# Kernel tuning notes

Hardware: AMD Instinct MI355X
Metric: run time of the kernel (lower is better)

Reference implementation:

```python
import jax, jax.numpy as jnp
import numpy as np

B = 4096        # batch (number of bags)
L = 64          # num_lookups per bag
NT = 4          # number of embedding tables
V = 500000      # rows per table
D = 128         # emb_dim
DENSE = 512     # dense feature dim
BOT = [512, 1024, 512, 128]
TOP = [D * (1 + NT), 1024, 512, 1]  # [640, 1024, 512, 1]


def _linear_params(key, dims):
    params = []
    for i in range(len(dims) - 1):
        din, dout = dims[i], dims[i + 1]
        kw, kb, key = jax.random.split(key, 3)
        sw = np.sqrt(2.0 / (din + dout)).astype(np.float32)
        sb = np.sqrt(1.0 / dout).astype(np.float32)
        params.append((sw * jax.random.normal(kw, (dout, din), jnp.float32),
                       sb * jax.random.normal(kb, (dout,), jnp.float32)))
    return params


def setup_inputs() -> dict:
    key = jax.random.key(0)
    k_dense, k_idx, k_tab, k_bot, k_top = jax.random.split(key, 5)
    inp = {}
    inp["x_dense"] = jax.random.normal(k_dense, (B, DENSE), jnp.float32)
    bound = float(np.sqrt(1.0 / V))
    inp["tables"] = jax.random.uniform(k_tab, (NT, V, D), jnp.float32, -bound, bound)
    bot = _linear_params(k_bot, BOT)
    top = _linear_params(k_top, TOP)
    inp["bw0"], inp["bb0"] = bot[0]
    inp["bw1"], inp["bb1"] = bot[1]
    inp["bw2"], inp["bb2"] = bot[2]
    inp["tw0"], inp["tb0"] = top[0]
    inp["tw1"], inp["tb1"] = top[1]
    inp["tw2"], inp["tb2"] = top[2]
    inp["x_indices"] = jax.random.randint(k_idx, (B * L, NT), 0, V, dtype=jnp.int32)
    inp["constant_offsets"] = jnp.arange(B, dtype=jnp.int32) * L  # offsets of each bag
    return inp


def reference(x_dense, tables, bw0, bb0, bw1, bb1, bw2, bb2,
              tw0, tb0, tw1, tb1, tw2, tb2, x_indices, constant_offsets):
    # bottom MLP: Linear+ReLU x3
    h = jax.nn.relu(x_dense @ bw0.T + bb0)
    h = jax.nn.relu(h @ bw1.T + bb1)
    bot_out = jax.nn.relu(h @ bw2.T + bb2)                     # [B, D]

    # EmbeddingBag (sum mode) per table, driven by offsets
    N = x_indices.shape[0]
    seg = jnp.searchsorted(constant_offsets, jnp.arange(N, dtype=constant_offsets.dtype),
                           side='right') - 1                    # [N] bag id per index
    gathered = jax.vmap(lambda tab, idx: tab[idx])(tables, x_indices.T)  # [NT, N, D]
    pooled = jax.vmap(lambda e: jax.ops.segment_sum(e, seg, num_segments=B))(gathered)  # [NT, B, D]

    # concat order: bottom MLP out, then tables 1..4 (columns 0..3)
    feat = jnp.concatenate([bot_out] + [pooled[t] for t in range(NT)], axis=1)  # [B, 640]

    # top MLP: ReLU, ReLU, Sigmoid
    z = jax.nn.relu(feat @ tw0.T + tb0)
    z = jax.nn.relu(z @ tw1.T + tb1)
    out = jax.nn.sigmoid(z @ tw2.T + tb2)                       # [B, 1]
    return out
```

## Files before the change

kernel.cpp:

```cpp
#include <hip/hip_runtime.h>
#include <hip/hip_bf16.h>
#include <cstdint>

#define B_BAGS 4096
#define L_LOOK 64
#define NT 4
#define V_ROWS 500000
#define D_EMB 128
#define FEAT 640

typedef _Float16 half8 __attribute__((ext_vector_type(8)));
typedef _Float16 half4 __attribute__((ext_vector_type(4)));
typedef float f32x4 __attribute__((ext_vector_type(4)));

#define GLOAD_LDS(g, l) __builtin_amdgcn_global_load_lds( \
    (const __attribute__((address_space(1))) void*)(g),   \
    (__attribute__((address_space(3))) void*)(l), 16, 0, 0)

template<int BM, int BN, bool RELU>
__device__ __forceinline__ void gemm_body(
    _Float16* lds, int bm, int bn,
    const _Float16* __restrict__ X, int ldx,
    const _Float16* __restrict__ W, int ldw,
    const float* __restrict__ bias,
    _Float16* __restrict__ Y, int ldy, int K)
{
    constexpr int BK = 64;
    constexpr int FM = BM / 32;
    constexpr int FN = BN / 32;
    constexpr int AI = BM * 8 / 256;
    constexpr int BI = BN * 8 / 256;

    _Float16* As = lds;
    _Float16* Bs = lds + BM * BK;

    const int tid  = threadIdx.x;
    const int lane = tid & 63;
    const int wave = tid >> 6;
    const int wm   = wave >> 1;
    const int wn   = wave & 1;
    const int q    = lane >> 4;
    const int r16  = lane & 15;

    f32x4 acc[FM][FN] = {};

    for (int k0 = 0; k0 < K; k0 += BK) {
#pragma unroll
        for (int i = 0; i < AI; ++i) {
            int L = i * 256 + tid;
            int row = L >> 3, sl = L & 7;
            const _Float16* src = X + (size_t)(bm + row) * ldx + k0 + ((sl ^ (row & 7)) * 8);
            GLOAD_LDS(src, As + (size_t)(i * 256 + wave * 64) * 8);
        }
#pragma unroll
        for (int j = 0; j < BI; ++j) {
            int L = j * 256 + tid;
            int row = L >> 3, sl = L & 7;
            const _Float16* src = W + (size_t)(bn + row) * ldw + k0 + ((sl ^ (row & 7)) * 8);
            GLOAD_LDS(src, Bs + (size_t)(j * 256 + wave * 64) * 8);
        }
        __syncthreads();

#pragma unroll
        for (int s = 0; s < 2; ++s) {
            half8 a[FM], b[FN];
#pragma unroll
            for (int i = 0; i < FM; ++i) {
                int R = wm * (BM / 2) + i * 16 + r16;
                int sl = (s * 4 + q) ^ (R & 7);
                a[i] = *(const half8*)(As + R * BK + sl * 8);
            }
#pragma unroll
            for (int j = 0; j < FN; ++j) {
                int R = wn * (BN / 2) + j * 16 + r16;
                int sl = (s * 4 + q) ^ (R & 7);
                b[j] = *(const half8*)(Bs + R * BK + sl * 8);
            }
#pragma unroll
            for (int i = 0; i < FM; ++i)
#pragma unroll
                for (int j = 0; j < FN; ++j)
                    acc[i][j] = __builtin_amdgcn_mfma_f32_16x16x32_f16(
                        a[i], b[j], acc[i][j], 0, 0, 0);
        }
        __syncthreads();
    }

#pragma unroll
    for (int i = 0; i < FM; ++i) {
        const int m0 = bm + wm * (BM / 2) + i * 16 + q * 4;
#pragma unroll
        for (int j = 0; j < FN; ++j) {
            const int n = bn + wn * (BN / 2) + j * 16 + r16;
            const float bv = bias[n];
#pragma unroll
            for (int e = 0; e < 4; ++e) {
                float o = acc[i][j][e] + bv;
                if (RELU) o = fmaxf(o, 0.f);
                Y[(size_t)(m0 + e) * ldy + n] = (_Float16)o;
            }
        }
    }
}

template<int BM, int BN, bool RELU>
__device__ __forceinline__ void gemm_body_f32(
    _Float16* lds, int bm, int bn,
    const float* __restrict__ X, int ldx,
    const float* __restrict__ W, int ldw,
    const float* __restrict__ bias,
    _Float16* __restrict__ Y, int ldy, int K)
{
    constexpr int BK = 64;
    constexpr int FM = BM / 32;
    constexpr int FN = BN / 32;
    constexpr int AI = BM * 8 / 256;
    constexpr int BI = BN * 8 / 256;

    _Float16* As = lds;
    _Float16* Bs = lds + BM * BK;

    const int tid  = threadIdx.x;
    const int lane = tid & 63;
    const int wave = tid >> 6;
    const int wm   = wave >> 1;
    const int wn   = wave & 1;
    const int q    = lane >> 4;
    const int r16  = lane & 15;

    f32x4 acc[FM][FN] = {};

    for (int k0 = 0; k0 < K; k0 += BK) {
#pragma unroll
        for (int i = 0; i < AI; ++i) {
            int S = i * 256 + tid;
            int row = S >> 3, c = S & 7;
            const float* src = X + (size_t)(bm + row) * ldx + k0 + c * 8;
            float4 v0 = *(const float4*)src;
            float4 v1 = *(const float4*)(src + 4);
            half8 h = { (_Float16)v0.x, (_Float16)v0.y, (_Float16)v0.z, (_Float16)v0.w,
                        (_Float16)v1.x, (_Float16)v1.y, (_Float16)v1.z, (_Float16)v1.w };
            *(half8*)(As + row * BK + ((c ^ (row & 7)) * 8)) = h;
        }
#pragma unroll
        for (int j = 0; j < BI; ++j) {
            int S = j * 256 + tid;
            int row = S >> 3, c = S & 7;
            const float* src = W + (size_t)(bn + row) * ldw + k0 + c * 8;
            float4 v0 = *(const float4*)src;
            float4 v1 = *(const float4*)(src + 4);
            half8 h = { (_Float16)v0.x, (_Float16)v0.y, (_Float16)v0.z, (_Float16)v0.w,
                        (_Float16)v1.x, (_Float16)v1.y, (_Float16)v1.z, (_Float16)v1.w };
            *(half8*)(Bs + row * BK + ((c ^ (row & 7)) * 8)) = h;
        }
        __syncthreads();

#pragma unroll
        for (int s = 0; s < 2; ++s) {
            half8 a[FM], b[FN];
#pragma unroll
            for (int i = 0; i < FM; ++i) {
                int R = wm * (BM / 2) + i * 16 + r16;
                int sl = (s * 4 + q) ^ (R & 7);
                a[i] = *(const half8*)(As + R * BK + sl * 8);
            }
#pragma unroll
            for (int j = 0; j < FN; ++j) {
                int R = wn * (BN / 2) + j * 16 + r16;
                int sl = (s * 4 + q) ^ (R & 7);
                b[j] = *(const half8*)(Bs + R * BK + sl * 8);
            }
#pragma unroll
            for (int i = 0; i < FM; ++i)
#pragma unroll
                for (int j = 0; j < FN; ++j)
                    acc[i][j] = __builtin_amdgcn_mfma_f32_16x16x32_f16(
                        a[i], b[j], acc[i][j], 0, 0, 0);
        }
        __syncthreads();
    }

#pragma unroll
    for (int i = 0; i < FM; ++i) {
        const int m0 = bm + wm * (BM / 2) + i * 16 + q * 4;
#pragma unroll
        for (int j = 0; j < FN; ++j) {
            const int n = bn + wn * (BN / 2) + j * 16 + r16;
            const float bv = bias[n];
#pragma unroll
            for (int e = 0; e < 4; ++e) {
                float o = acc[i][j][e] + bv;
                if (RELU) o = fmaxf(o, 0.f);
                Y[(size_t)(m0 + e) * ldy + n] = (_Float16)o;
            }
        }
    }
}

__device__ __forceinline__ void emb_body(
    int bag,
    const float* __restrict__ tables,
    const int*   __restrict__ idx,
    _Float16*    __restrict__ feat)
{
    const int wave = threadIdx.x >> 6;
    const int lane = threadIdx.x & 63;
    const int l5   = lane >> 5;
    const int c    = lane & 31;

    const int my_idx = idx[((size_t)bag * L_LOOK + lane) * NT + wave];
    const float* tab = tables + (size_t)wave * V_ROWS * D_EMB;

    float4 acc = {0.f, 0.f, 0.f, 0.f};
#pragma unroll 16
    for (int j = 0; j < 32; ++j) {
        int r = __shfl(my_idx, 2 * j + l5, 64);
        float4 v = ((const float4*)(tab + (size_t)r * D_EMB))[c];
        acc.x += v.x; acc.y += v.y; acc.z += v.z; acc.w += v.w;
    }
    acc.x += __shfl_xor(acc.x, 32, 64);
    acc.y += __shfl_xor(acc.y, 32, 64);
    acc.z += __shfl_xor(acc.z, 32, 64);
    acc.w += __shfl_xor(acc.w, 32, 64);
    if (l5 == 0) {
        half4 h = { (_Float16)acc.x, (_Float16)acc.y, (_Float16)acc.z, (_Float16)acc.w };
        *(half4*)(feat + (size_t)bag * FEAT + D_EMB + wave * D_EMB + c * 4) = h;
    }
}

__device__ __forceinline__ void top2_body(
    int row,
    const _Float16* __restrict__ Z,
    const _Float16* __restrict__ w,
    const float* __restrict__ bsc,
    float* __restrict__ out)
{
    const int lane = threadIdx.x & 63;
    half8 z  = *(const half8*)(Z + (size_t)row * 512 + lane * 8);
    half8 wv = *(const half8*)(w + lane * 8);
    float s = 0.f;
#pragma unroll
    for (int i = 0; i < 8; ++i) s += (float)z[i] * (float)wv[i];
#pragma unroll
    for (int off = 32; off > 0; off >>= 1) s += __shfl_down(s, off, 64);
    if (lane == 0) {
        float x = s + bsc[0];
        out[row] = 1.f / (1.f + expf(-x));
    }
}

struct GD {
    const _Float16* X; const _Float16* W; const float* bias; _Float16* Y;
    int ldx, ldw, ldy, K, m0, mTiles;
};

__global__ __launch_bounds__(256, 3) void mega(
    GD gA, int nA, GD gB, int nB,
    int embBase, int embCount,
    const float* __restrict__ tables, const int* __restrict__ idx,
    _Float16* __restrict__ feat,
    const _Float16* __restrict__ z1, const _Float16* __restrict__ tw2h,
    const float* __restrict__ tb2, float* __restrict__ outp,
    int t2Base)
{
    __shared__ __align__(16) _Float16 lds[(128 + 128) * 64];
    int bid = blockIdx.x;
    if (bid < nA) {
        gemm_body<128, 128, true>(lds, gA.m0 + (bid % gA.mTiles) * 128,
                                  (bid / gA.mTiles) * 128,
                                  gA.X, gA.ldx, gA.W, gA.ldw, gA.bias,
                                  gA.Y, gA.ldy, gA.K);
        return;
    }
    bid -= nA;
    if (bid < nB) {
        gemm_body<128, 128, true>(lds, gB.m0 + (bid % gB.mTiles) * 128,
                                  (bid / gB.mTiles) * 128,
                                  gB.X, gB.ldx, gB.W, gB.ldw, gB.bias,
                                  gB.Y, gB.ldy, gB.K);
        return;
    }
    bid -= nB;
    if (bid < embCount) {
        emb_body(embBase + bid, tables, idx, feat);
        return;
    }
    bid -= embCount;
    top2_body(t2Base + bid * 4 + (threadIdx.x >> 6), z1, tw2h, tb2, outp);
}

struct CvtRest {
    const float* src[5];
    _Float16*    dst[5];
    int          n4[5];
};

__global__ __launch_bounds__(256, 3) void fused1(
    const float* __restrict__ X, const float* __restrict__ W,
    const float* __restrict__ bias, _Float16* __restrict__ Y,
    CvtRest cvt,
    int embCount,
    const float* __restrict__ tables, const int* __restrict__ idx,
    _Float16* __restrict__ feat)
{
    __shared__ __align__(16) _Float16 lds[(128 + 128) * 64];
    int bid = blockIdx.x;
    if (bid < 256) {
        gemm_body_f32<128, 128, true>(lds, (bid & 31) * 128, (bid >> 5) * 128,
                                      X, 512, W, 512, bias, Y, 1024, 512);
        return;
    }
    bid -= 256;
    if (bid < 64) {
        const int t0 = bid * 256 + threadIdx.x;
        const int stride = 64 * 256;
#pragma unroll
        for (int t = 0; t < 5; ++t) {
            const float4* s = (const float4*)cvt.src[t];
            half4* d = (half4*)cvt.dst[t];
            for (int i = t0; i < cvt.n4[t]; i += stride) {
                float4 v = s[i];
                half4 h = { (_Float16)v.x, (_Float16)v.y, (_Float16)v.z, (_Float16)v.w };
                d[i] = h;
            }
        }
        return;
    }
    emb_body(bid - 64, tables, idx, feat);
}

extern "C" void kernel_launch(void* const* d_in, const int* in_sizes, int n_in,
                              void* d_out, int out_size, void* d_ws, size_t ws_size,
                              hipStream_t stream) {
    const float* x_dense = (const float*)d_in[0];
    const float* tables  = (const float*)d_in[1];
    const float* bw0 = (const float*)d_in[2];
    const float* bb0 = (const float*)d_in[3];
    const float* bw1 = (const float*)d_in[4];
    const float* bb1 = (const float*)d_in[5];
    const float* bw2 = (const float*)d_in[6];
    const float* bb2 = (const float*)d_in[7];
    const float* tw0 = (const float*)d_in[8];
    const float* tb0 = (const float*)d_in[9];
    const float* tw1 = (const float*)d_in[10];
    const float* tb1 = (const float*)d_in[11];
    const float* tw2 = (const float*)d_in[12];
    const float* tb2 = (const float*)d_in[13];
    const int*   x_idx = (const int*)d_in[14];
    float* out = (float*)d_out;

    char* p = (char*)d_ws;
    auto alloc = [&](size_t bytes) {
        char* r = p; p += (bytes + 255) & ~(size_t)255; return r;
    };
    _Float16* bw1h = (_Float16*)alloc((size_t)512 * 1024 * 2);
    _Float16* bw2h = (_Float16*)alloc((size_t)128 * 512 * 2);
    _Float16* tw0h = (_Float16*)alloc((size_t)1024 * 640 * 2);
    _Float16* tw1h = (_Float16*)alloc((size_t)512 * 1024 * 2);
    _Float16* tw2h = (_Float16*)alloc((size_t)512 * 2);
    _Float16* h0h  = (_Float16*)alloc((size_t)4096 * 1024 * 2);
    _Float16* h1h  = (_Float16*)alloc((size_t)4096 * 512 * 2);
    _Float16* feat = (_Float16*)alloc((size_t)4096 * 640 * 2);
    _Float16* z0h  = (_Float16*)alloc((size_t)4096 * 1024 * 2);
    _Float16* z1h  = (_Float16*)alloc((size_t)4096 * 512 * 2);

    CvtRest cr;
    cr.src[0] = bw1; cr.dst[0] = bw1h; cr.n4[0] = 512 * 1024 / 4;
    cr.src[1] = bw2; cr.dst[1] = bw2h; cr.n4[1] = 128 * 512 / 4;
    cr.src[2] = tw0; cr.dst[2] = tw0h; cr.n4[2] = 1024 * 640 / 4;
    cr.src[3] = tw1; cr.dst[3] = tw1h; cr.n4[3] = 512 * 1024 / 4;
    cr.src[4] = tw2; cr.dst[4] = tw2h; cr.n4[4] = 512 / 4;

    dim3 blk(256);

    GD g2;
    g2.X = h0h; g2.W = bw1h; g2.bias = bb1; g2.Y = h1h;
    g2.ldx = 1024; g2.ldw = 1024; g2.ldy = 512; g2.K = 1024; g2.m0 = 0; g2.mTiles = 32;

    GD g3;
    g3.X = h1h; g3.W = bw2h; g3.bias = bb2; g3.Y = feat;
    g3.ldx = 512; g3.ldw = 512; g3.ldy = 640; g3.K = 512; g3.m0 = 0; g3.mTiles = 32;

    GD t0a;
    t0a.X = feat; t0a.W = tw0h; t0a.bias = tb0; t0a.Y = z0h;
    t0a.ldx = 640; t0a.ldw = 640; t0a.ldy = 1024; t0a.K = 640; t0a.m0 = 0; t0a.mTiles = 16;

    GD t0b = t0a; t0b.m0 = 2048;

    GD t1a;
    t1a.X = z0h; t1a.W = tw1h; t1a.bias = tb1; t1a.Y = z1h;
    t1a.ldx = 1024; t1a.ldw = 1024; t1a.ldy = 512; t1a.K = 1024; t1a.m0 = 0; t1a.mTiles = 16;

    GD t1b = t1a; t1b.m0 = 2048;

    fused1<<<dim3(256 + 64 + 1792), blk, 0, stream>>>(
        x_dense, bw0, bb0, h0h, cr, 1792, tables, x_idx, feat);

    mega<<<dim3(128 + 1280), blk, 0, stream>>>(
        g2, 128, g2, 0, 1792, 1280, tables, x_idx, feat,
        z1h, tw2h, tb2, out, 0);

    mega<<<dim3(32 + 512), blk, 0, stream>>>(
        g3, 32, g3, 0, 3072, 512, tables, x_idx, feat,
        z1h, tw2h, tb2, out, 0);

    mega<<<dim3(128 + 512), blk, 0, stream>>>(
        t0a, 128, t0a, 0, 3584, 512, tables, x_idx, feat,
        z1h, tw2h, tb2, out, 0);

    mega<<<dim3(128 + 64), blk, 0, stream>>>(
        t0b, 128, t1a, 64, 0, 0, tables, x_idx, feat,
        z1h, tw2h, tb2, out, 0);

    mega<<<dim3(64 + 512), blk, 0, stream>>>(
        t1b, 64, t1b, 0, 0, 0, tables, x_idx, feat,
        z1h, tw2h, tb2, out, 0);

    mega<<<dim3(512), blk, 0, stream>>>(
        t1b, 0, t1b, 0, 0, 0, tables, x_idx, feat,
        z1h, tw2h, tb2, out, 2048);
}
```

Measured before the change: 180.5 us.

## Rebalance embedding work across launches and run top MLP as plain GEMM kernels

Moves more embedding-bag blocks into the first three launches so every embedding row is pooled before the top MLP starts. The top MLP layers then run as dedicated full-size GEMM launches instead of being split into half-batch pieces interleaved with embedding work. The final sigmoid dot product also gets its own kernel. This cuts the launch count and removes the half-batch splits, but gives up overlapping top-MLP GEMMs with embedding gathers.

Result: faster. 167.4 us (-7.3%).

```diff
diff --git a/kernel.cpp b/kernel.cpp
--- a/kernel.cpp
+++ b/kernel.cpp
@@ -228,40 +228,16 @@
     }
 }
 
-__device__ __forceinline__ void top2_body(
-    int row,
-    const _Float16* __restrict__ Z,
-    const _Float16* __restrict__ w,
-    const float* __restrict__ bsc,
-    float* __restrict__ out)
-{
-    const int lane = threadIdx.x & 63;
-    half8 z  = *(const half8*)(Z + (size_t)row * 512 + lane * 8);
-    half8 wv = *(const half8*)(w + lane * 8);
-    float s = 0.f;
-#pragma unroll
-    for (int i = 0; i < 8; ++i) s += (float)z[i] * (float)wv[i];
-#pragma unroll
-    for (int off = 32; off > 0; off >>= 1) s += __shfl_down(s, off, 64);
-    if (lane == 0) {
-        float x = s + bsc[0];
-        out[row] = 1.f / (1.f + expf(-x));
-    }
-}
-
 struct GD {
     const _Float16* X; const _Float16* W; const float* bias; _Float16* Y;
     int ldx, ldw, ldy, K, m0, mTiles;
 };
 
 __global__ __launch_bounds__(256, 3) void mega(
-    GD gA, int nA, GD gB, int nB,
+    GD gA, int nA,
     int embBase, int embCount,
     const float* __restrict__ tables, const int* __restrict__ idx,
-    _Float16* __restrict__ feat,
-    const _Float16* __restrict__ z1, const _Float16* __restrict__ tw2h,
-    const float* __restrict__ tb2, float* __restrict__ outp,
-    int t2Base)
+    _Float16* __restrict__ feat)
 {
     __shared__ __align__(16) _Float16 lds[(128 + 128) * 64];
     int bid = blockIdx.x;
@@ -273,20 +249,7 @@
         return;
     }
     bid -= nA;
-    if (bid < nB) {
-        gemm_body<128, 128, true>(lds, gB.m0 + (bid % gB.mTiles) * 128,
-                                  (bid / gB.mTiles) * 128,
-                                  gB.X, gB.ldx, gB.W, gB.ldw, gB.bias,
-                                  gB.Y, gB.ldy, gB.K);
-        return;
-    }
-    bid -= nB;
-    if (bid < embCount) {
-        emb_body(embBase + bid, tables, idx, feat);
-        return;
-    }
-    bid -= embCount;
-    top2_body(t2Base + bid * 4 + (threadIdx.x >> 6), z1, tw2h, tb2, outp);
+    emb_body(embBase + bid, tables, idx, feat);
 }
 
 struct CvtRest {
@@ -299,7 +262,6 @@
     const float* __restrict__ X, const float* __restrict__ W,
     const float* __restrict__ bias, _Float16* __restrict__ Y,
     CvtRest cvt,
-    int embCount,
     const float* __restrict__ tables, const int* __restrict__ idx,
     _Float16* __restrict__ feat)
 {
@@ -327,6 +289,41 @@
         return;
     }
     emb_body(bid - 64, tables, idx, feat);
+}
+
+template<int BM, int BN, bool RELU>
+__global__ __launch_bounds__(256, 3) void gemm_h(
+    const _Float16* __restrict__ X, int ldx,
+    const _Float16* __restrict__ W, int ldw,
+    const float* __restrict__ bias,
+    _Float16* __restrict__ Y, int ldy,
+    int K)
+{
+    __shared__ __align__(16) _Float16 lds[(BM + BN) * 64];
+    gemm_body<BM, BN, RELU>(lds, blockIdx.y * BM, blockIdx.x * BN,
+                            X, ldx, W, ldw, bias, Y, ldy, K);
+}
+
+__global__ __launch_bounds__(256) void top2_h(
+    const _Float16* __restrict__ Z,
+    const _Float16* __restrict__ w,
+    const float* __restrict__ bsc,
+    float* __restrict__ out)
+{
+    const int row  = blockIdx.x * 4 + (threadIdx.x >> 6);
+    const int lane = threadIdx.x & 63;
+
+    half8 z  = *(const half8*)(Z + (size_t)row * 512 + lane * 8);
+    half8 wv = *(const half8*)(w + lane * 8);
+    float s = 0.f;
+#pragma unroll
+    for (int i = 0; i < 8; ++i) s += (float)z[i] * (float)wv[i];
+#pragma unroll
+    for (int off = 32; off > 0; off >>= 1) s += __shfl_down(s, off, 64);
+    if (lane == 0) {
+        float x = s + bsc[0];
+        out[row] = 1.f / (1.f + expf(-x));
+    }
 }
 
 extern "C" void kernel_launch(void* const* d_in, const int* in_sizes, int n_in,
@@ -381,42 +378,20 @@
     g3.X = h1h; g3.W = bw2h; g3.bias = bb2; g3.Y = feat;
     g3.ldx = 512; g3.ldw = 512; g3.ldy = 640; g3.K = 512; g3.m0 = 0; g3.mTiles = 32;
 
-    GD t0a;
-    t0a.X = feat; t0a.W = tw0h; t0a.bias = tb0; t0a.Y = z0h;
-    t0a.ldx = 640; t0a.ldw = 640; t0a.ldy = 1024; t0a.K = 640; t0a.m0 = 0; t0a.mTiles = 16;
-
-    GD t0b = t0a; t0b.m0 = 2048;
-
-    GD t1a;
-    t1a.X = z0h; t1a.W = tw1h; t1a.bias = tb1; t1a.Y = z1h;
-    t1a.ldx = 1024; t1a.ldw = 1024; t1a.ldy = 512; t1a.K = 1024; t1a.m0 = 0; t1a.mTiles = 16;
-
-    GD t1b = t1a; t1b.m0 = 2048;
-
-    fused1<<<dim3(256 + 64 + 1792), blk, 0, stream>>>(
-        x_dense, bw0, bb0, h0h, cr, 1792, tables, x_idx, feat);
+    fused1<<<dim3(256 + 64 + 2048), blk, 0, stream>>>(
+        x_dense, bw0, bb0, h0h, cr, tables, x_idx, feat);
 
     mega<<<dim3(128 + 1280), blk, 0, stream>>>(
-        g2, 128, g2, 0, 1792, 1280, tables, x_idx, feat,
-        z1h, tw2h, tb2, out, 0);
-
-    mega<<<dim3(32 + 512), blk, 0, stream>>>(
-        g3, 32, g3, 0, 3072, 512, tables, x_idx, feat,
-        z1h, tw2h, tb2, out, 0);
-
-    mega<<<dim3(128 + 512), blk, 0, stream>>>(
-        t0a, 128, t0a, 0, 3584, 512, tables, x_idx, feat,
-        z1h, tw2h, tb2, out, 0);
-
-    mega<<<dim3(128 + 64), blk, 0, stream>>>(
-        t0b, 128, t1a, 64, 0, 0, tables, x_idx, feat,
-        z1h, tw2h, tb2, out, 0);
-
-    mega<<<dim3(64 + 512), blk, 0, stream>>>(
-        t1b, 64, t1b, 0, 0, 0, tables, x_idx, feat,
-        z1h, tw2h, tb2, out, 0);
-
-    mega<<<dim3(512), blk, 0, stream>>>(
-        t1b, 0, t1b, 0, 0, 0, tables, x_idx, feat,
-        z1h, tw2h, tb2, out, 2048);
-}
+        g2, 128, 2048, 1280, tables, x_idx, feat);
+
+    mega<<<dim3(32 + 768), blk, 0, stream>>>(
+        g3, 32, 3328, 768, tables, x_idx, feat);
+
+    gemm_h<128, 128, true><<<dim3(8, 32), blk, 0, stream>>>(
+        feat, 640, tw0h, 640, tb0, z0h, 1024, 640);
+
+    gemm_h<128, 128, true><<<dim3(4, 32), blk, 0, stream>>>(
+        z0h, 1024, tw1h, 1024, tb1, z1h, 512, 1024);
+
+    top2_h<<<dim3(1024), blk, 0, stream>>>(z1h, tw2h, tb2, out);
+}
```
